# Performance work log

Measured on AMD Instinct MI355X. Metric: run time of the kernel, lower is better.

## Reference

```python
import jax, jax.numpy as jnp
import numpy as np

KH = KW = 3
STRIDE = 1
PAD = 1
DIL = 1
DG = 1  # deformable groups


def setup_inputs() -> dict:
    key = jax.random.key(0)
    k1, k2, k3, k4 = jax.random.split(key, 4)
    B, C, H, W = 8, 256, 64, 64
    OC = 256
    x = jax.random.normal(k1, (B, C, H, W), dtype=jnp.float32)
    offset = jax.random.normal(k2, (B, 2 * DG * KH * KW, H, W), dtype=jnp.float32)
    mask = jax.random.uniform(k3, (B, DG * KH * KW, H, W), dtype=jnp.float32)
    stdv = 1.0 / np.sqrt(C * KH * KW)
    weight = jax.random.uniform(k4, (OC, C, KH, KW), dtype=jnp.float32, minval=-stdv, maxval=stdv)
    bias = jnp.zeros((OC,), dtype=jnp.float32)
    return {"x": x, "offset": offset, "mask": mask, "weight": weight, "bias": bias}


def _deform_sample(x, py, px):
    """Bilinear sample x (B,C,H,W) at fractional locations py/px (B,K,Ho,Wo),
    zero outside the image. Returns (B,C,K,Ho,Wo)."""
    B, C, H, W = x.shape
    xf = x.reshape(B, C, H * W)
    y0 = jnp.floor(py)
    x0 = jnp.floor(px)
    wy1 = py - y0
    wx1 = px - x0

    def corner(yc, xc, w):
        valid = (yc >= 0) & (yc < H) & (xc >= 0) & (xc < W)
        yi = jnp.clip(yc, 0, H - 1).astype(jnp.int32)
        xi = jnp.clip(xc, 0, W - 1).astype(jnp.int32)
        idx = (yi * W + xi).reshape(B, -1)  # (B, K*Ho*Wo)
        g = jax.vmap(lambda xb, ib: xb[:, ib])(xf, idx)  # (B,C,K*Ho*Wo)
        g = g.reshape(B, C, *yc.shape[1:])
        return g * (w * valid)[:, None]

    return (
        corner(y0, x0, (1 - wy1) * (1 - wx1))
        + corner(y0, x0 + 1, (1 - wy1) * wx1)
        + corner(y0 + 1, x0, wy1 * (1 - wx1))
        + corner(y0 + 1, x0 + 1, wy1 * wx1)
    )


def reference(x, offset, mask, weight, bias):
    B, C, H, W = x.shape
    OC = weight.shape[0]
    K = KH * KW
    Ho = (H + 2 * PAD - DIL * (KH - 1) - 1) // STRIDE + 1
    Wo = (W + 2 * PAD - DIL * (KW - 1) - 1) // STRIDE + 1

    # base sampling grid: top-left anchor + kernel taps
    oy = jnp.arange(Ho, dtype=jnp.float32) * STRIDE - PAD  # (Ho,)
    ox = jnp.arange(Wo, dtype=jnp.float32) * STRIDE - PAD  # (Wo,)
    ky = jnp.repeat(jnp.arange(KH, dtype=jnp.float32) * DIL, KW)  # (K,)
    kx = jnp.tile(jnp.arange(KW, dtype=jnp.float32) * DIL, KH)    # (K,)

    # offsets: channels laid out as (dg, k, [dy, dx]); dg == 1 here
    off = offset.reshape(B, DG, K, 2, Ho, Wo)
    py = ky[None, :, None, None] + oy[None, None, :, None] + off[:, 0, :, 0]  # (B,K,Ho,Wo)
    px = kx[None, :, None, None] + ox[None, None, None, :] + off[:, 0, :, 1]

    cols = _deform_sample(x, py, px)  # (B,C,K,Ho,Wo)
    cols = cols * mask.reshape(B, 1, K, Ho, Wo)  # modulation

    out = jnp.einsum('bckhw,ock->bohw', cols, weight.reshape(OC, C, K))
    return out + bias[None, :, None, None]
```

## Files before the change

### kernel.cpp

```cpp
#include <hip/hip_runtime.h>
#include <stdint.h>


typedef __attribute__((ext_vector_type(8))) _Float16 half8;
typedef __attribute__((ext_vector_type(2))) __fp16 fp16x2;
typedef __attribute__((ext_vector_type(4))) float floatx4;
typedef __attribute__((ext_vector_type(4))) unsigned int uintx4;

#define MFMA16(A, B, C) __builtin_amdgcn_mfma_f32_16x16x32_f16(A, B, C, 0, 0, 0)

__device__ __forceinline__ unsigned short f16_bits_rne(float v) {
    _Float16 hf = (_Float16)v;
    union { _Float16 f; unsigned short s; } a; a.f = hf;
    return a.s;
}

__device__ __forceinline__ void pack8(const float* vals, uintx4& pkH) {
#pragma unroll
    for (int p = 0; p < 4; p++) {
        fp16x2 h = __builtin_amdgcn_cvt_pkrtz(vals[2 * p], vals[2 * p + 1]);
        union { fp16x2 v; unsigned int u; } ch; ch.v = h;
        pkH[p] = ch.u;
    }
}

__device__ __forceinline__ void mk_coords(int tap, int ho, int wo,
    float offy, float offx, float m,
    int& yx00, int& yx01, int& yx10, int& yx11,
    float& w00, float& w01, float& w10, float& w11) {
    float py = (float)(tap / 3) + (float)(ho - 1) + offy;
    float px = (float)(tap % 3) + (float)(wo - 1) + offx;
    float y0f = floorf(py), x0f = floorf(px);
    float wy1 = py - y0f, wx1 = px - x0f;
    float wy0 = 1.f - wy1, wx0 = 1.f - wx1;
    int y0 = (int)y0f, x0 = (int)x0f, y1 = y0 + 1, x1 = x0 + 1;
    bool vy0 = (y0 >= 0) && (y0 < 64), vy1 = (y1 >= 0) && (y1 < 64);
    bool vx0 = (x0 >= 0) && (x0 < 64), vx1 = (x1 >= 0) && (x1 < 64);
    int cy0 = min(max(y0, 0), 63), cy1 = min(max(y1, 0), 63);
    int cx0 = min(max(x0, 0), 63), cx1 = min(max(x1, 0), 63);
    yx00 = cy0 * 64 + cx0; yx01 = cy0 * 64 + cx1;
    yx10 = cy1 * 64 + cx0; yx11 = cy1 * 64 + cx1;
    w00 = wy0 * wx0 * m * ((vy0 && vx0) ? 1.f : 0.f);
    w01 = wy0 * wx1 * m * ((vy0 && vx1) ? 1.f : 0.f);
    w10 = wy1 * wx0 * m * ((vy1 && vx0) ? 1.f : 0.f);
    w11 = wy1 * wx1 * m * ((vy1 && vx1) ? 1.f : 0.f);
}

__global__ __launch_bounds__(256) void k_prep_xt(const float* __restrict__ x,
                                                 unsigned short* __restrict__ xtfh) {
    __shared__ float T[64][65];
    const int blk = blockIdx.x;
    const int b = blk >> 8;
    const int ct = (blk >> 6) & 3;
    const int tt = blk & 63;
    const int t = threadIdx.x;
    const int jj = t & 63, i4 = t >> 6;
    const float* xb = x + ((size_t)b << 20);
#pragma unroll 4
    for (int ii = 0; ii < 16; ii++) {
        int i = ii * 4 + i4;
        T[i][jj] = xb[((size_t)(ct * 64 + i) << 12) + tt * 64 + jj];
    }
    __syncthreads();
    unsigned short* ob = xtfh + ((size_t)b << 20);
#pragma unroll 4
    for (int ii = 0; ii < 16; ii++) {
        int jo = ii * 4 + i4;
        ob[((size_t)(tt * 64 + jo) << 8) + ct * 64 + jj] = f16_bits_rne(T[jj][jo]);
    }
}

__global__ __launch_bounds__(256) void k_prep_w2(const float* __restrict__ w,
                                                 unsigned short* __restrict__ bw2) {
    int tid = blockIdx.x * 256 + threadIdx.x;
    int j = tid & 7;
    int oc = (tid >> 3) & 255;
    int c = (tid >> 11) & 3;
    int step = tid >> 13;
    int ktap = step >> 3;
    int ch = ((step & 7) << 5) + (c << 3) + j;
    float v = w[oc * 2304 + ch * 9 + ktap] * 64.f;
    bw2[tid] = f16_bits_rne(v);
}

__global__ __launch_bounds__(256, 2) void k_dcn_v13(
    const float* __restrict__ offset,
    const float* __restrict__ mask,
    const float* __restrict__ bias,
    const unsigned short* __restrict__ xtfh,
    const unsigned short* __restrict__ bw2,
    float* __restrict__ out)
{
    __shared__ __align__(16) unsigned short Bs[9 * 2112];

    const int t = threadIdx.x;
    const int tile = blockIdx.x;
    const int b = tile & 7;
    const int ho = tile >> 3;

    const int lane = t & 63, wid = t >> 6, quad = lane >> 4, l15 = lane & 15;
    const int gpos = t >> 2, gseg = t & 3;
    const int wo = gpos;
    const int spos = (ho << 6) + wo;
    const unsigned short* xh = xtfh + ((size_t)b << 20);

    const unsigned short* aBase = bw2 + quad * 2048 + (((wid << 6) + l15) << 3);

    floatx4 acc[4][4];
#pragma unroll
    for (int i = 0; i < 4; i++)
#pragma unroll
        for (int j = 0; j < 4; j++) acc[i][j] = (floatx4){0.f, 0.f, 0.f, 0.f};

    float om0[9], om1[9], omm[9];
#pragma unroll
    for (int tp = 0; tp < 9; ++tp) {
        om0[tp] = offset[((size_t)(b * 18 + 2 * tp) << 12) + spos];
        om1[tp] = offset[((size_t)(b * 18 + 2 * tp + 1) << 12) + spos];
        omm[tp] = mask[((size_t)(b * 9 + tp) << 12) + spos];
    }

    half8 aCur[4], aNxt[4];
    half8 crnA[4], crnB[4];
    int yxs[2][4];
    float wss[2][4];

#define MK(TP, S) do { mk_coords((TP), ho, wo, om0[TP], om1[TP], omm[TP],   \
        yxs[S][0], yxs[S][1], yxs[S][2], yxs[S][3],                         \
        wss[S][0], wss[S][1], wss[S][2], wss[S][3]); } while (0)

#define LOAD_CRN(DST, S, C) do {                                            \
    const int cb = ((C) << 5) + (gseg << 3);                                \
    DST[0] = *(const half8*)(xh + ((size_t)yxs[S][0] << 8) + cb);           \
    DST[1] = *(const half8*)(xh + ((size_t)yxs[S][1] << 8) + cb);           \
    DST[2] = *(const half8*)(xh + ((size_t)yxs[S][2] << 8) + cb);           \
    DST[3] = *(const half8*)(xh + ((size_t)yxs[S][3] << 8) + cb);           \
    } while (0)

#define GEN_WRITE(CRN, S, SLOT) do {                                        \
    float vals[8];                                                          \
    _Pragma("unroll")                                                       \
    for (int q = 0; q < 8; q++) {                                           \
        vals[q] = wss[S][0] * (float)CRN[0][q] + wss[S][1] * (float)CRN[1][q] \
                + wss[S][2] * (float)CRN[2][q] + wss[S][3] * (float)CRN[3][q];\
    }                                                                       \
    uintx4 pkH;                                                             \
    pack8(vals, pkH);                                                       \
    unsigned short* bp = Bs + (SLOT) * 2112 + gseg * 528 + (gpos << 3);     \
    *(uintx4*)bp = pkH;                                                     \
    } while (0)

#define LOAD_A(DST, STEP) do {                                              \
    const unsigned short* ap = aBase + (size_t)(STEP) * 8192;               \
    _Pragma("unroll")                                                       \
    for (int i = 0; i < 4; i++) DST[i] = *(const half8*)(ap + i * 128);     \
    } while (0)

#define MFMA_STEP(SLOT, AREG) do {                                          \
    const unsigned short* Bp = Bs + (SLOT) * 2112 + quad * 528;             \
    half8 bH[4];                                                            \
    _Pragma("unroll")                                                       \
    for (int j = 0; j < 4; j++)                                             \
        bH[j] = *(const half8*)(Bp + (((j << 4) + l15) << 3));              \
    _Pragma("unroll")                                                       \
    for (int i = 0; i < 4; i++)                                             \
    _Pragma("unroll")                                                       \
        for (int j = 0; j < 4; j++)                                         \
            acc[i][j] = MFMA16(AREG[i], bH[j], acc[i][j]);                  \
    } while (0)

    for (int c = 0; c < 8; ++c) {
        MK(0, 0);
        LOAD_CRN(crnA, 0, c);
#pragma unroll
        for (int tp = 0; tp < 9; ++tp) {
            if (tp < 8) {
                if ((tp & 1) == 0) { MK(tp + 1, 1); LOAD_CRN(crnB, 1, c); }
                else               { MK(tp + 1, 0); LOAD_CRN(crnA, 0, c); }
            }
            if ((tp & 1) == 0) GEN_WRITE(crnA, 0, tp);
            else               GEN_WRITE(crnB, 1, tp);
        }
        __syncthreads();

        LOAD_A(aCur, c);
#pragma unroll
        for (int tp = 0; tp < 9; ++tp) {
            if (tp < 8) {
                if ((tp & 1) == 0) LOAD_A(aNxt, (tp + 1) * 8 + c);
                else               LOAD_A(aCur, (tp + 1) * 8 + c);
            }
            if ((tp & 1) == 0) MFMA_STEP(tp, aCur);
            else               MFMA_STEP(tp, aNxt);
        }
        __syncthreads();
    }

    float* outb = out + ((size_t)b << 20);
    const int posbase = ho << 6;
#pragma unroll
    for (int i = 0; i < 4; i++) {
        const int ocb = (wid << 6) + (i << 4) + (quad << 2);
#pragma unroll
        for (int r = 0; r < 4; r++) {
            const float bv = bias[ocb + r];
#pragma unroll
            for (int j = 0; j < 4; j++) {
                const int pos = posbase + (j << 4) + l15;
                outb[((size_t)(ocb + r) << 12) + pos] = acc[i][j][r] * 0.015625f + bv;
            }
        }
    }
#undef MK
#undef LOAD_CRN
#undef GEN_WRITE
#undef LOAD_A
#undef MFMA_STEP
}

__device__ __forceinline__ void split_f16_bits(float v, unsigned int& h, unsigned int& l) {
    _Float16 hf = (_Float16)v;
    float hff = (float)hf;
    _Float16 lf = (_Float16)(v - hff);
    union { _Float16 f; unsigned short s; } a2, b2;
    a2.f = hf; b2.f = lf;
    h = a2.s; l = b2.s;
}
__device__ __forceinline__ void split_pack8(const float* vals, uintx4& pkH, uintx4& pkL) {
#pragma unroll
    for (int p = 0; p < 4; p++) {
        float v0 = vals[2 * p], v1 = vals[2 * p + 1];
        fp16x2 h = __builtin_amdgcn_cvt_pkrtz(v0, v1);
        float h0 = (float)h[0], h1 = (float)h[1];
        fp16x2 l = __builtin_amdgcn_cvt_pkrtz(v0 - h0, v1 - h1);
        union { fp16x2 v; unsigned int u; } ch, cl;
        ch.v = h; cl.v = l;
        pkH[p] = ch.u;
        pkL[p] = cl.u;
    }
}

__global__ __launch_bounds__(256, 2) void k_dcn_fb(
    const float* __restrict__ x, const float* __restrict__ offset,
    const float* __restrict__ mask, const float* __restrict__ weight,
    const float* __restrict__ bias, float* __restrict__ out)
{
    __shared__ __align__(16) unsigned short AsH[256 * 40];
    __shared__ __align__(16) unsigned short AsL[256 * 40];
    __shared__ __align__(16) unsigned short BsH[64 * 40];
    __shared__ __align__(16) unsigned short BsL[64 * 40];
    __shared__ int cY[64][4];
    __shared__ float cW[64][4];

    const int t = threadIdx.x;
    const int tile = blockIdx.x;
    const int b = tile >> 6;
    const int ho = tile & 63;
    const int lane = t & 63, wid = t >> 6, quad = lane >> 4, l15 = lane & 15;
    const int gpos = t >> 2, gseg = t & 3;

    floatx4 acc[4][4];
#pragma unroll
    for (int i = 0; i < 4; i++)
#pragma unroll
        for (int j = 0; j < 4; j++) acc[i][j] = (floatx4){0.f, 0.f, 0.f, 0.f};

    for (int ktap = 0; ktap < 9; ++ktap) {
        __syncthreads();
        if (t < 64) {
            int wo = t;
            int spos = (ho << 6) + wo;
            float offy = offset[(((size_t)(b * 18 + 2 * ktap)) << 12) + spos];
            float offx = offset[(((size_t)(b * 18 + 2 * ktap + 1)) << 12) + spos];
            float m = mask[(((size_t)(b * 9 + ktap)) << 12) + spos];
            int c0, c1, c2, c3; float u0, u1, u2, u3;
            mk_coords(ktap, ho, wo, offy, offx, m, c0, c1, c2, c3, u0, u1, u2, u3);
            cY[t][0] = c0; cY[t][1] = c1; cY[t][2] = c2; cY[t][3] = c3;
            cW[t][0] = u0; cW[t][1] = u1; cW[t][2] = u2; cW[t][3] = u3;
        }
        __syncthreads();
        const int yx00 = cY[gpos][0], yx01 = cY[gpos][1];
        const int yx10 = cY[gpos][2], yx11 = cY[gpos][3];
        const float w00 = cW[gpos][0], w01 = cW[gpos][1];
        const float w10 = cW[gpos][2], w11 = cW[gpos][3];

        for (int cs = 0; cs < 8; ++cs) {
            const int c0 = cs << 5;
            {
                const float* wp = weight + (size_t)t * 2304 + (size_t)c0 * 9 + ktap;
#pragma unroll
                for (int kj = 0; kj < 32; kj += 2) {
                    unsigned int h0, l0u, h1, l1u;
                    split_f16_bits(wp[kj * 9] * 64.f, h0, l0u);
                    split_f16_bits(wp[kj * 9 + 9] * 64.f, h1, l1u);
                    *(unsigned int*)&AsH[t * 40 + kj] = h0 | (h1 << 16);
                    *(unsigned int*)&AsL[t * 40 + kj] = l0u | (l1u << 16);
                }
            }
            {
                const int cb = c0 + (gseg << 3);
                const float* xg = x + ((size_t)b << 20);
                float vals[8];
#pragma unroll
                for (int j = 0; j < 8; j++) {
                    const float* xc = xg + ((size_t)(cb + j) << 12);
                    vals[j] = w00 * xc[yx00] + w01 * xc[yx01] +
                              w10 * xc[yx10] + w11 * xc[yx11];
                }
                uintx4 pkH, pkL;
                split_pack8(vals, pkH, pkL);
                *(uintx4*)&BsH[gpos * 40 + (gseg << 3)] = pkH;
                *(uintx4*)&BsL[gpos * 40 + (gseg << 3)] = pkL;
            }
            __syncthreads();
            half8 aH[4], aL[4], bH[4], bL[4];
#pragma unroll
            for (int i = 0; i < 4; i++) {
                const int rowA = (wid << 6) + (i << 4) + l15;
                aH[i] = *(const half8*)&AsH[rowA * 40 + (quad << 3)];
                aL[i] = *(const half8*)&AsL[rowA * 40 + (quad << 3)];
            }
#pragma unroll
            for (int j = 0; j < 4; j++) {
                const int rowB = (j << 4) + l15;
                bH[j] = *(const half8*)&BsH[rowB * 40 + (quad << 3)];
                bL[j] = *(const half8*)&BsL[rowB * 40 + (quad << 3)];
            }
#pragma unroll
            for (int i = 0; i < 4; i++)
#pragma unroll
                for (int j = 0; j < 4; j++) {
                    acc[i][j] = MFMA16(aH[i], bH[j], acc[i][j]);
                    acc[i][j] = MFMA16(aL[i], bH[j], acc[i][j]);
                    acc[i][j] = MFMA16(aH[i], bL[j], acc[i][j]);
                }
            __syncthreads();
        }
    }
    float* outb = out + ((size_t)b << 20);
    const int posbase = ho << 6;
#pragma unroll
    for (int i = 0; i < 4; i++) {
        const int ocb = (wid << 6) + (i << 4) + (quad << 2);
#pragma unroll
        for (int r = 0; r < 4; r++) {
            const float bv = bias[ocb + r];
#pragma unroll
            for (int j = 0; j < 4; j++) {
                const int pos = posbase + (j << 4) + l15;
                outb[((size_t)(ocb + r) << 12) + pos] = acc[i][j][r] * 0.015625f + bv;
            }
        }
    }
}

extern "C" void kernel_launch(void* const* d_in, const int* in_sizes, int n_in,
                              void* d_out, int out_size, void* d_ws, size_t ws_size,
                              hipStream_t stream) {
    const float* x      = (const float*)d_in[0];
    const float* offset = (const float*)d_in[1];
    const float* mask   = (const float*)d_in[2];
    const float* weight = (const float*)d_in[3];
    const float* bias   = (const float*)d_in[4];
    float* out = (float*)d_out;

    const size_t xtf_bytes = (size_t)8 * 4096 * 256 * 2;
    const size_t bw2_elems = (size_t)72 * 8192;
    const size_t need = xtf_bytes + bw2_elems * 2;

    if (ws_size >= need) {
        unsigned short* xtfh = (unsigned short*)d_ws;
        unsigned short* bw2 = (unsigned short*)((char*)d_ws + xtf_bytes);
        k_prep_xt<<<2048, 256, 0, stream>>>(x, xtfh);
        k_prep_w2<<<(int)(bw2_elems / 256), 256, 0, stream>>>(weight, bw2);
        k_dcn_v13<<<512, 256, 0, stream>>>(offset, mask, bias, xtfh, bw2, out);
    } else {
        k_dcn_fb<<<512, 256, 0, stream>>>(x, offset, mask, weight, bias, out);
    }
}
```

Baseline: 155.6 us.

## Use 512-thread blocks splitting taps and output channels; merge prep kernels

The main DCN kernel now runs 512 threads per block. Two thread groups split the nine bilinear-sampling taps between them (even and odd taps), and eight waves each own 32 output channels instead of four waves owning 64. Accumulator and A-register footprint per thread is halved, which is meant to allow more resident waves and better latency hiding. The two prep kernels (x transpose and weight repack) are fused into a single launch to save one kernel launch. In exchange, the extra ninth-tap slot leaves the second group idle during part of the sampling phase, and more waves compete for the same LDS tile.

```diff
diff --git a/kernel.cpp b/kernel.cpp
--- a/kernel.cpp
+++ b/kernel.cpp
@@ -46,44 +46,45 @@
     w11 = wy1 * wx1 * m * ((vy1 && vx1) ? 1.f : 0.f);
 }
 
-__global__ __launch_bounds__(256) void k_prep_xt(const float* __restrict__ x,
-                                                 unsigned short* __restrict__ xtfh) {
+__global__ __launch_bounds__(256) void k_prep(const float* __restrict__ x,
+                                              const float* __restrict__ w,
+                                              unsigned short* __restrict__ xtfh,
+                                              unsigned short* __restrict__ bw2) {
     __shared__ float T[64][65];
     const int blk = blockIdx.x;
-    const int b = blk >> 8;
-    const int ct = (blk >> 6) & 3;
-    const int tt = blk & 63;
     const int t = threadIdx.x;
-    const int jj = t & 63, i4 = t >> 6;
-    const float* xb = x + ((size_t)b << 20);
+    if (blk < 2048) {
+        const int b = blk >> 8;
+        const int ct = (blk >> 6) & 3;
+        const int tt = blk & 63;
+        const int jj = t & 63, i4 = t >> 6;
+        const float* xb = x + ((size_t)b << 20);
 #pragma unroll 4
-    for (int ii = 0; ii < 16; ii++) {
-        int i = ii * 4 + i4;
-        T[i][jj] = xb[((size_t)(ct * 64 + i) << 12) + tt * 64 + jj];
-    }
-    __syncthreads();
-    unsigned short* ob = xtfh + ((size_t)b << 20);
+        for (int ii = 0; ii < 16; ii++) {
+            int i = ii * 4 + i4;
+            T[i][jj] = xb[((size_t)(ct * 64 + i) << 12) + tt * 64 + jj];
+        }
+        __syncthreads();
+        unsigned short* ob = xtfh + ((size_t)b << 20);
 #pragma unroll 4
-    for (int ii = 0; ii < 16; ii++) {
-        int jo = ii * 4 + i4;
-        ob[((size_t)(tt * 64 + jo) << 8) + ct * 64 + jj] = f16_bits_rne(T[jj][jo]);
-    }
-}
-
-__global__ __launch_bounds__(256) void k_prep_w2(const float* __restrict__ w,
-                                                 unsigned short* __restrict__ bw2) {
-    int tid = blockIdx.x * 256 + threadIdx.x;
-    int j = tid & 7;
-    int oc = (tid >> 3) & 255;
-    int c = (tid >> 11) & 3;
-    int step = tid >> 13;
-    int ktap = step >> 3;
-    int ch = ((step & 7) << 5) + (c << 3) + j;
-    float v = w[oc * 2304 + ch * 9 + ktap] * 64.f;
-    bw2[tid] = f16_bits_rne(v);
-}
-
-__global__ __launch_bounds__(256, 2) void k_dcn_v13(
+        for (int ii = 0; ii < 16; ii++) {
+            int jo = ii * 4 + i4;
+            ob[((size_t)(tt * 64 + jo) << 8) + ct * 64 + jj] = f16_bits_rne(T[jj][jo]);
+        }
+    } else {
+        int tid = (blk - 2048) * 256 + t;
+        int j = tid & 7;
+        int oc = (tid >> 3) & 255;
+        int c = (tid >> 11) & 3;
+        int step = tid >> 13;
+        int ktap = step >> 3;
+        int ch = ((step & 7) << 5) + (c << 3) + j;
+        float v = w[oc * 2304 + ch * 9 + ktap] * 64.f;
+        bw2[tid] = f16_bits_rne(v);
+    }
+}
+
+__global__ __launch_bounds__(512, 4) void k_dcn_v14(
     const float* __restrict__ offset,
     const float* __restrict__ mask,
     const float* __restrict__ bias,
@@ -98,51 +99,57 @@
     const int b = tile & 7;
     const int ho = tile >> 3;
 
-    const int lane = t & 63, wid = t >> 6, quad = lane >> 4, l15 = lane & 15;
-    const int gpos = t >> 2, gseg = t & 3;
+    const int lane = t & 63, w8 = t >> 6, quad = (t >> 4) & 3, l15 = t & 15;
+    const int grp = t >> 8;
+    const int th = t & 255;
+    const int gpos = th >> 2, gseg = th & 3;
     const int wo = gpos;
     const int spos = (ho << 6) + wo;
     const unsigned short* xh = xtfh + ((size_t)b << 20);
 
-    const unsigned short* aBase = bw2 + quad * 2048 + (((wid << 6) + l15) << 3);
-
-    floatx4 acc[4][4];
-#pragma unroll
-    for (int i = 0; i < 4; i++)
+    const unsigned short* aBase = bw2 + quad * 2048 + (((w8 << 5) + l15) << 3);
+
+    floatx4 acc[2][4];
+#pragma unroll
+    for (int i = 0; i < 2; i++)
 #pragma unroll
         for (int j = 0; j < 4; j++) acc[i][j] = (floatx4){0.f, 0.f, 0.f, 0.f};
 
-    float om0[9], om1[9], omm[9];
-#pragma unroll
-    for (int tp = 0; tp < 9; ++tp) {
-        om0[tp] = offset[((size_t)(b * 18 + 2 * tp) << 12) + spos];
-        om1[tp] = offset[((size_t)(b * 18 + 2 * tp + 1) << 12) + spos];
-        omm[tp] = mask[((size_t)(b * 9 + tp) << 12) + spos];
-    }
-
-    half8 aCur[4], aNxt[4];
+    float om0s[5], om1s[5], omms[5];
+#pragma unroll
+    for (int s = 0; s < 5; ++s) {
+        int tap = 2 * s + grp; if (tap > 8) tap = 8;
+        om0s[s] = offset[((size_t)(b * 18 + 2 * tap) << 12) + spos];
+        om1s[s] = offset[((size_t)(b * 18 + 2 * tap + 1) << 12) + spos];
+        omms[s] = mask[((size_t)(b * 9 + tap) << 12) + spos];
+    }
+
+    half8 aCur[2], aNxt[2];
     half8 crnA[4], crnB[4];
     int yxs[2][4];
     float wss[2][4];
 
-#define MK(TP, S) do { mk_coords((TP), ho, wo, om0[TP], om1[TP], omm[TP],   \
-        yxs[S][0], yxs[S][1], yxs[S][2], yxs[S][3],                         \
-        wss[S][0], wss[S][1], wss[S][2], wss[S][3]); } while (0)
-
-#define LOAD_CRN(DST, S, C) do {                                            \
+#define MK(S, SET) do { int _tap = 2 * (S) + grp; if (_tap > 8) _tap = 8;   \
+    mk_coords(_tap, ho, wo, om0s[S], om1s[S], omms[S],                      \
+        yxs[SET][0], yxs[SET][1], yxs[SET][2], yxs[SET][3],                 \
+        wss[SET][0], wss[SET][1], wss[SET][2], wss[SET][3]); } while (0)
+
+#define LOAD_CRN(DST, SET, C) do {                                          \
     const int cb = ((C) << 5) + (gseg << 3);                                \
-    DST[0] = *(const half8*)(xh + ((size_t)yxs[S][0] << 8) + cb);           \
-    DST[1] = *(const half8*)(xh + ((size_t)yxs[S][1] << 8) + cb);           \
-    DST[2] = *(const half8*)(xh + ((size_t)yxs[S][2] << 8) + cb);           \
-    DST[3] = *(const half8*)(xh + ((size_t)yxs[S][3] << 8) + cb);           \
+    DST[0] = *(const half8*)(xh + ((size_t)yxs[SET][0] << 8) + cb);         \
+    DST[1] = *(const half8*)(xh + ((size_t)yxs[SET][1] << 8) + cb);         \
+    DST[2] = *(const half8*)(xh + ((size_t)yxs[SET][2] << 8) + cb);         \
+    DST[3] = *(const half8*)(xh + ((size_t)yxs[SET][3] << 8) + cb);         \
     } while (0)
 
-#define GEN_WRITE(CRN, S, SLOT) do {                                        \
+#define GEN_WRITE(CRN, SET, SLOT) do {                                      \
     float vals[8];                                                          \
     _Pragma("unroll")                                                       \
     for (int q = 0; q < 8; q++) {                                           \
-        vals[q] = wss[S][0] * (float)CRN[0][q] + wss[S][1] * (float)CRN[1][q] \
-                + wss[S][2] * (float)CRN[2][q] + wss[S][3] * (float)CRN[3][q];\
+        vals[q] = wss[SET][0] * (float)CRN[0][q]                            \
+                + wss[SET][1] * (float)CRN[1][q]                            \
+                + wss[SET][2] * (float)CRN[2][q]                            \
+                + wss[SET][3] * (float)CRN[3][q];                           \
     }                                                                       \
     uintx4 pkH;                                                             \
     pack8(vals, pkH);                                                       \
@@ -152,8 +159,8 @@
 
 #define LOAD_A(DST, STEP) do {                                              \
     const unsigned short* ap = aBase + (size_t)(STEP) * 8192;               \
-    _Pragma("unroll")                                                       \
-    for (int i = 0; i < 4; i++) DST[i] = *(const half8*)(ap + i * 128);     \
+    DST[0] = *(const half8*)ap;                                             \
+    DST[1] = *(const half8*)(ap + 128);                                     \
     } while (0)
 
 #define MFMA_STEP(SLOT, AREG) do {                                          \
@@ -163,7 +170,7 @@
     for (int j = 0; j < 4; j++)                                             \
         bH[j] = *(const half8*)(Bp + (((j << 4) + l15) << 3));              \
     _Pragma("unroll")                                                       \
-    for (int i = 0; i < 4; i++)                                             \
+    for (int i = 0; i < 2; i++)                                             \
     _Pragma("unroll")                                                       \
         for (int j = 0; j < 4; j++)                                         \
             acc[i][j] = MFMA16(AREG[i], bH[j], acc[i][j]);                  \
@@ -173,13 +180,16 @@
         MK(0, 0);
         LOAD_CRN(crnA, 0, c);
 #pragma unroll
-        for (int tp = 0; tp < 9; ++tp) {
-            if (tp < 8) {
-                if ((tp & 1) == 0) { MK(tp + 1, 1); LOAD_CRN(crnB, 1, c); }
-                else               { MK(tp + 1, 0); LOAD_CRN(crnA, 0, c); }
-            }
-            if ((tp & 1) == 0) GEN_WRITE(crnA, 0, tp);
-            else               GEN_WRITE(crnB, 1, tp);
+        for (int s = 0; s < 5; ++s) {
+            if (s < 4) {
+                if ((s & 1) == 0) { MK(s + 1, 1); LOAD_CRN(crnB, 1, c); }
+                else              { MK(s + 1, 0); LOAD_CRN(crnA, 0, c); }
+            }
+            const int slot = 2 * s + grp;
+            if (s < 4 || grp == 0) {
+                if ((s & 1) == 0) GEN_WRITE(crnA, 0, slot);
+                else              GEN_WRITE(crnB, 1, slot);
+            }
         }
         __syncthreads();
 
@@ -199,8 +209,8 @@
     float* outb = out + ((size_t)b << 20);
     const int posbase = ho << 6;
 #pragma unroll
-    for (int i = 0; i < 4; i++) {
-        const int ocb = (wid << 6) + (i << 4) + (quad << 2);
+    for (int i = 0; i < 2; i++) {
+        const int ocb = (w8 << 5) + (i << 4) + (quad << 2);
 #pragma unroll
         for (int r = 0; r < 4; r++) {
             const float bv = bias[ocb + r];
@@ -371,9 +381,8 @@
     if (ws_size >= need) {
         unsigned short* xtfh = (unsigned short*)d_ws;
         unsigned short* bw2 = (unsigned short*)((char*)d_ws + xtf_bytes);
-        k_prep_xt<<<2048, 256, 0, stream>>>(x, xtfh);
-        k_prep_w2<<<(int)(bw2_elems / 256), 256, 0, stream>>>(weight, bw2);
-        k_dcn_v13<<<512, 256, 0, stream>>>(offset, mask, bias, xtfh, bw2, out);
+        k_prep<<<2048 + 2304, 256, 0, stream>>>(x, weight, xtfh, bw2);
+        k_dcn_v14<<<512, 512, 0, stream>>>(offset, mask, bias, xtfh, bw2, out);
     } else {
         k_dcn_fb<<<512, 256, 0, stream>>>(x, offset, mask, weight, bias, out);
     }
```

Measured after the change: 148.0 us. 4.8% less time.
